# Kernel optimization log

Measured on AMD Instinct MI355X. Metric: run time of the kernel, lower is better.

Reference implementation:

```python
import jax, jax.numpy as jnp
import numpy as np
from jax import lax

POINTS = 512  # number of FPS-sampled centroids
KNN = 16      # neighbors per centroid


def setup_inputs() -> dict:
    key = jax.random.key(0)
    # [B, N, 3+C]: first 3 channels are xyz coordinates, rest are features
    x = jax.random.normal(key, (8, 16384, 16), dtype=jnp.float32)
    return {"x": x}


def _furthest_point_sample(xyz, npoint):
    """Standard FPS (seeded at index 0, as in the pointnet2 CUDA op).
    xyz: [B, N, 3] -> idx: [B, npoint] int32."""
    B, N, _ = xyz.shape

    def step(carry, _):
        min_d, last = carry
        last_pt = jnp.take_along_axis(xyz, last[:, None, None], axis=1)  # [B,1,3]
        d = jnp.sum((xyz - last_pt) ** 2, axis=-1)                        # [B,N]
        min_d = jnp.minimum(min_d, d)
        nxt = jnp.argmax(min_d, axis=-1).astype(jnp.int32)
        return (min_d, nxt), nxt

    first = jnp.zeros((B,), dtype=jnp.int32)
    init = (jnp.full((B, N), 1e10, dtype=xyz.dtype), first)
    _, rest = lax.scan(step, init, None, length=npoint - 1)  # [npoint-1, B]
    return jnp.concatenate([first[:, None], rest.T], axis=1)  # [B, npoint]


def _index_points(points, idx):
    """points: [B,N,C], idx: [B,S] or [B,S,K] -> gathered [*idx.shape, C]."""
    B = points.shape[0]
    flat = idx.reshape(B, -1)                                  # [B, S*K]
    out = jnp.take_along_axis(points, flat[:, :, None], axis=1)
    return out.reshape(*idx.shape, points.shape[-1])


def reference(x):
    # FPS over coordinates only
    idx = _furthest_point_sample(x[:, :, :3], POINTS)          # [B, P]
    sampled = _index_points(x, idx)                             # [B, P, 3+C]
    s = sampled[:, :, :3]
    p = x[:, :, :3]
    # squared euclidean distance: ||s||^2 + ||p||^2 - 2 s.p  -> [B, P, N]
    dist = (jnp.sum(s * s, axis=-1)[:, :, None]
            + jnp.sum(p * p, axis=-1)[:, None, :]
            - 2.0 * jnp.einsum('bpc,bnc->bpn', s, p))
    # full argsort then slice, matching distances.argsort()[:, :, :knn]
    knn_idx = jnp.argsort(dist, axis=-1)[:, :, :KNN]            # [B, P, K]
    return _index_points(x, knn_idx)                            # [B, P, K, 3+C]
```

## Files before the change

kernel.cpp:

```cpp
#include <hip/hip_runtime.h>
#include <hip/hip_bf16.h>
#include <stdint.h>

#define B_      8
#define N_      16384
#define NPOINT  512
#define KNN_    16
#define C_      16

__device__ __forceinline__ float fmulrn(float a, float b){ return __fmul_rn(a,b); }
__device__ __forceinline__ float faddrn(float a, float b){ return __fadd_rn(a,b); }
__device__ __forceinline__ float fsubrn(float a, float b){ return __fsub_rn(a,b); }

__device__ __forceinline__ uint32_t umax_(uint32_t a, uint32_t b){ return a > b ? a : b; }

__device__ __forceinline__ uint32_t row16_max(uint32_t x){
    uint32_t t;
    t = (uint32_t)__builtin_amdgcn_update_dpp((int)x, (int)x, 0x111, 0xf, 0xf, false); x = umax_(x, t);
    t = (uint32_t)__builtin_amdgcn_update_dpp((int)x, (int)x, 0x112, 0xf, 0xf, false); x = umax_(x, t);
    t = (uint32_t)__builtin_amdgcn_update_dpp((int)x, (int)x, 0x114, 0xf, 0xf, false); x = umax_(x, t);
    t = (uint32_t)__builtin_amdgcn_update_dpp((int)x, (int)x, 0x118, 0xf, 0xf, false); x = umax_(x, t);
    return x;
}

__device__ __forceinline__ uint32_t wave_max_uniform(uint32_t x){
    x = row16_max(x);
    uint32_t a = (uint32_t)__builtin_amdgcn_readlane((int)x, 15);
    uint32_t b = (uint32_t)__builtin_amdgcn_readlane((int)x, 31);
    uint32_t c = (uint32_t)__builtin_amdgcn_readlane((int)x, 47);
    uint32_t d = (uint32_t)__builtin_amdgcn_readlane((int)x, 63);
    return umax_(umax_(a, b), umax_(c, d));
}

__device__ __forceinline__ unsigned long long quad_max_u64(unsigned long long k){
    uint32_t lo = (uint32_t)k, hi = (uint32_t)(k >> 32);
    {
        uint32_t olo = (uint32_t)__builtin_amdgcn_update_dpp((int)lo, (int)lo, 0xB1, 0xf, 0xf, false);
        uint32_t ohi = (uint32_t)__builtin_amdgcn_update_dpp((int)hi, (int)hi, 0xB1, 0xf, 0xf, false);
        bool take = (ohi > hi) || (ohi == hi && olo > lo);
        hi = take ? ohi : hi; lo = take ? olo : lo;
    }
    {
        uint32_t olo = (uint32_t)__builtin_amdgcn_update_dpp((int)lo, (int)lo, 0x4E, 0xf, 0xf, false);
        uint32_t ohi = (uint32_t)__builtin_amdgcn_update_dpp((int)hi, (int)hi, 0x4E, 0xf, 0xf, false);
        bool take = (ohi > hi) || (ohi == hi && olo > lo);
        hi = take ? ohi : hi; lo = take ? olo : lo;
    }
    return ((unsigned long long)hi << 32) | lo;
}

__global__ void prep_kernel(const float* __restrict__ x, float4* __restrict__ pts){
    int i = blockIdx.x * blockDim.x + threadIdx.x;
    if (i >= B_ * N_) return;
    const float4* x4 = (const float4*)x;
    float4 q = x4[(size_t)i * 4];
    float p2 = faddrn(faddrn(fmulrn(q.x,q.x), fmulrn(q.y,q.y)), fmulrn(q.z,q.z));
    pts[i] = make_float4(q.x, q.y, q.z, p2);
}

#define FPS_NB   4
#define MBOX_N   (B_ * NPOINT * FPS_NB)
__global__ void zero_part_kernel(unsigned long long* __restrict__ part){
    int i = blockIdx.x * blockDim.x + threadIdx.x;
    if (i < MBOX_N) part[i] = 0ULL;
}

#define FPS_T    1024
#define FPS_NW   (FPS_T/64)
#define SLICE    (N_ / FPS_NB)
#define FOR_S4(F) F(0) F(1) F(2) F(3)

__global__ void __launch_bounds__(FPS_T)
fps_kernel_mb(const float4* __restrict__ pts, float4* __restrict__ s_out,
              unsigned long long* __restrict__ part){
    __shared__ float2   xy[SLICE];
    __shared__ uint32_t red_v[2][FPS_NW];
    __shared__ uint32_t red_i[2][FPS_NW];

    const int b    = blockIdx.x & 7;
    const int blk  = blockIdx.x >> 3;
    const int tid  = threadIdx.x;
    const int lane = tid & 63;
    const int wv   = tid >> 6;
    const int base = blk * SLICE;
    const float4* P = pts + (size_t)b * N_;
    unsigned long long* mbox = part + ((size_t)b * NPOINT) * FPS_NB;

#define DECL_S(s) float z##s, md##s;
    FOR_S4(DECL_S)
#undef DECL_S

#define INIT_S(s) { float4 q = P[base + (s) * FPS_T + tid]; \
        xy[(s) * FPS_T + tid] = make_float2(q.x, q.y); \
        z##s = q.z; md##s = 1e10f; }
    FOR_S4(INIT_S)
#undef INIT_S

    float lx, ly, lz;
    {
        float4 q0 = P[0];
        lx = q0.x; ly = q0.y; lz = q0.z;
        if (blk == 0 && tid == 0) s_out[(size_t)b * NPOINT + 0] = q0;
    }
    __syncthreads();

    for (int it = 1; it < NPOINT; ++it){
        float    bv = -1.0f;
        uint32_t bi = 0;
#define DO_S(s) { \
        float2 c = xy[(s) * FPS_T + tid]; \
        float dx = fsubrn(c.x, lx); \
        float dy = fsubrn(c.y, ly); \
        float dz = fsubrn(z##s, lz); \
        float d  = faddrn(faddrn(fmulrn(dx,dx), fmulrn(dy,dy)), fmulrn(dz,dz)); \
        md##s = fminf(md##s, d); \
        if (md##s > bv){ bv = md##s; bi = (uint32_t)(base + (s) * FPS_T + tid); } }
        FOR_S4(DO_S)
#undef DO_S

        uint32_t vb    = __float_as_uint(bv);
        uint32_t gmaxw = wave_max_uniform(vb);
        uint32_t gidxw = wave_max_uniform((vb == gmaxw) ? ~bi : 0u);
        const int par = it & 1;
        if (lane == 0){ red_v[par][wv] = gmaxw; red_i[par][wv] = gidxw; }
        __syncthreads();
        uint32_t rv = red_v[par][lane & 15];
        uint32_t ri = red_i[par][lane & 15];
        uint32_t gv = (uint32_t)__builtin_amdgcn_readlane((int)row16_max(rv), 15);
        uint32_t gn = (uint32_t)__builtin_amdgcn_readlane(
                          (int)row16_max((rv == gv) ? ri : 0u), 15);
        unsigned long long kblk = ((unsigned long long)gv << 32) | gn;

        unsigned long long* slotp = mbox + (size_t)it * FPS_NB;
        if (tid == 0)
            __hip_atomic_store(&slotp[blk], kblk, __ATOMIC_RELAXED,
                               __HIP_MEMORY_SCOPE_AGENT);
        unsigned long long v = 0;
        int guard = 0;
        for (;;){
            if (v == 0)
                v = __hip_atomic_load(&slotp[lane & 3], __ATOMIC_RELAXED,
                                      __HIP_MEMORY_SCOPE_AGENT);
            if (__all(v != 0ULL)) break;
            if (++guard > (1 << 20)) return;
        }
        unsigned long long kmax = quad_max_u64(v);
        uint32_t gi  = ~((uint32_t)kmax);
        uint32_t giu = (uint32_t)__builtin_amdgcn_readfirstlane((int)gi);
        giu &= (uint32_t)(N_ - 1);
        float4 q = P[giu];
        lx = q.x; ly = q.y; lz = q.z;
        if (blk == 0 && tid == 0) s_out[(size_t)b * NPOINT + it] = q;
    }
}

#define KT       1024
#define KNN_T    512

__global__ void __launch_bounds__(KNN_T)
__attribute__((amdgpu_waves_per_eu(4, 4)))
knn_kernel(const float* __restrict__ x,
           const float4* __restrict__ pts,
           const float4* __restrict__ s_arr,
           float* __restrict__ out){
    __shared__ float4 tile[KT];

    const int wv   = threadIdx.x >> 6;
    const int lane = threadIdx.x & 63;
    const int blk  = blockIdx.x;
    const int b    = blk >> 6;
    const int p    = ((blk & 63) << 3) | wv;

    const float4 s = s_arr[(size_t)b * NPOINT + p];
    const float sx = s.x, sy = s.y, sz = s.z, s2 = s.w;
    const float4* P = pts + (size_t)b * N_;

#define FOR_V(F) F(0) F(1) F(2) F(3) F(4) F(5) F(6) F(7) \
                 F(8) F(9) F(10) F(11) F(12) F(13) F(14) F(15)
#define DECLV(t) unsigned long long v##t = ~0ULL;
    FOR_V(DECLV)
#undef DECLV

#define PROC(q, n) { \
        float dot = faddrn(faddrn(fmulrn(sz, (q).z), fmulrn(sy, (q).y)), fmulrn(sx, (q).x)); \
        float d = fsubrn(faddrn(s2, (q).w), fmulrn(2.0f, dot)); \
        uint32_t bits = __float_as_uint(d); \
        uint32_t key  = bits ^ (((uint32_t)((int32_t)bits >> 31)) | 0x80000000u); \
        unsigned long long c = ((unsigned long long)key << 32) | (uint32_t)(n); \
        if (c < v15){ \
            bool lt0=c<v0,  lt1=c<v1,  lt2=c<v2,  lt3=c<v3; \
            bool lt4=c<v4,  lt5=c<v5,  lt6=c<v6,  lt7=c<v7; \
            bool lt8=c<v8,  lt9=c<v9,  lt10=c<v10, lt11=c<v11; \
            bool lt12=c<v12, lt13=c<v13, lt14=c<v14; \
            v15 = lt14 ? v14 : c; \
            v14 = lt14 ? (lt13 ? v13 : c) : v14; \
            v13 = lt13 ? (lt12 ? v12 : c) : v13; \
            v12 = lt12 ? (lt11 ? v11 : c) : v12; \
            v11 = lt11 ? (lt10 ? v10 : c) : v11; \
            v10 = lt10 ? (lt9  ? v9  : c) : v10; \
            v9  = lt9  ? (lt8  ? v8  : c) : v9;  \
            v8  = lt8  ? (lt7  ? v7  : c) : v8;  \
            v7  = lt7  ? (lt6  ? v6  : c) : v7;  \
            v6  = lt6  ? (lt5  ? v5  : c) : v6;  \
            v5  = lt5  ? (lt4  ? v4  : c) : v5;  \
            v4  = lt4  ? (lt3  ? v3  : c) : v4;  \
            v3  = lt3  ? (lt2  ? v2  : c) : v3;  \
            v2  = lt2  ? (lt1  ? v1  : c) : v2;  \
            v1  = lt1  ? (lt0  ? v0  : c) : v1;  \
            v0  = lt0  ? c : v0; \
        } }

    for (int t = 0; t < N_/KT; ++t){
        float4 a0 = P[t*KT + threadIdx.x];
        float4 a1 = P[t*KT + threadIdx.x + KNN_T];
        __syncthreads();
        tile[threadIdx.x]          = a0;
        tile[threadIdx.x + KNN_T]  = a1;
        __syncthreads();
        #pragma unroll 4
        for (int g = 0; g < KT/64; ++g){
            const int n = t*KT + (g << 6) + lane;
            float4 q = tile[(g << 6) + lane];
            PROC(q, n)
        }
    }
#undef PROC

    uint32_t myidx = 0;
    const int myr = lane >> 2;
    #pragma unroll 1
    for (int r = 0; r < KNN_; ++r){
        unsigned long long h = v0;
        unsigned long long g = h;
        #pragma unroll
        for (int off = 1; off < 64; off <<= 1){
            unsigned long long o = __shfl_xor(g, off, 64);
            if (o < g) g = o;
        }
        if (h == g){
            v0=v1; v1=v2; v2=v3; v3=v4; v4=v5; v5=v6; v6=v7; v7=v8;
            v8=v9; v9=v10; v10=v11; v11=v12; v12=v13; v13=v14; v14=v15;
            v15=~0ULL;
        }
        if (myr == r) myidx = (uint32_t)g;
    }
    myidx &= (uint32_t)(N_ - 1);

    const int c4 = lane & 3;
    const float4* X4 = (const float4*)x;
    float4 valq = X4[((size_t)b * N_ + myidx) * 4 + c4];
    float4* O4 = (float4*)out;
    O4[(((size_t)b * NPOINT + p) * KNN_ + myr) * 4 + c4] = valq;
}

extern "C" void kernel_launch(void* const* d_in, const int* in_sizes, int n_in,
                              void* d_out, int out_size, void* d_ws, size_t ws_size,
                              hipStream_t stream) {
    const float* x = (const float*)d_in[0];
    float* out = (float*)d_out;

    const size_t pts_bytes  = (size_t)B_ * N_ * sizeof(float4);
    const size_t s_bytes    = (size_t)B_ * NPOINT * sizeof(float4);
    const size_t part_bytes = (size_t)MBOX_N * sizeof(unsigned long long);
    if (ws_size < pts_bytes + s_bytes + part_bytes) return;
    float4* pts   = (float4*)d_ws;
    float4* s_arr = (float4*)((char*)d_ws + pts_bytes);
    unsigned long long* part =
        (unsigned long long*)((char*)d_ws + pts_bytes + s_bytes);

    prep_kernel<<<(B_*N_ + 255)/256, 256, 0, stream>>>(x, pts);
    zero_part_kernel<<<(MBOX_N + 255)/256, 256, 0, stream>>>(part);
    fps_kernel_mb<<<B_*FPS_NB, FPS_T, 0, stream>>>(pts, s_arr, part);
    knn_kernel<<<(B_*NPOINT)/8, KNN_T, 0, stream>>>(x, pts, s_arr, out);
}
```

Baseline: 1.018 ms.

## Fuse FPS and KNN into one kernel with progress-flag streaming

Merges the FPS and KNN kernels into a single launch. The first 32 blocks run FPS and publish each sampled centroid plus a per-batch progress counter with release atomics. The remaining blocks wait on that counter until their 16 centroids exist, then run the KNN top-16 scan, so KNN work overlaps the long serial FPS loop. KNN blocks grow to 1024 threads (16 centroids each), and the shared tile load is cut to one float4 per thread. Correctness depends on all FPS blocks being resident before spinning KNN blocks fill the GPU, and the larger fused block may raise register pressure for the KNN path.

Result: slower. 2.141 ms (+110.3%).

```diff
diff --git a/kernel.cpp b/kernel.cpp
--- a/kernel.cpp
+++ b/kernel.cpp
@@ -60,9 +60,10 @@
 
 #define FPS_NB   4
 #define MBOX_N   (B_ * NPOINT * FPS_NB)
+#define ZERO_N   (MBOX_N + 8)
 __global__ void zero_part_kernel(unsigned long long* __restrict__ part){
     int i = blockIdx.x * blockDim.x + threadIdx.x;
-    if (i < MBOX_N) part[i] = 0ULL;
+    if (i < ZERO_N) part[i] = 0ULL;
 }
 
 #define FPS_T    1024
@@ -70,109 +71,138 @@
 #define SLICE    (N_ / FPS_NB)
 #define FOR_S4(F) F(0) F(1) F(2) F(3)
 
-__global__ void __launch_bounds__(FPS_T)
-fps_kernel_mb(const float4* __restrict__ pts, float4* __restrict__ s_out,
-              unsigned long long* __restrict__ part){
+#define FUSE_FPS_BLOCKS (B_ * FPS_NB)
+#define KNN_RPB  16
+#define FUSE_KNN_BLOCKS (B_ * NPOINT / KNN_RPB)
+#define KT       1024
+
+__global__ void __launch_bounds__(1024, 8)
+fused_kernel(const float4* __restrict__ pts,
+             unsigned long long* __restrict__ sarr,
+             unsigned long long* __restrict__ part,
+             unsigned int* __restrict__ prog,
+             const float* __restrict__ x,
+             float* __restrict__ out){
     __shared__ float2   xy[SLICE];
     __shared__ uint32_t red_v[2][FPS_NW];
     __shared__ uint32_t red_i[2][FPS_NW];
-
-    const int b    = blockIdx.x & 7;
-    const int blk  = blockIdx.x >> 3;
+    __shared__ float4   tile[KT];
+
     const int tid  = threadIdx.x;
     const int lane = tid & 63;
     const int wv   = tid >> 6;
-    const int base = blk * SLICE;
-    const float4* P = pts + (size_t)b * N_;
-    unsigned long long* mbox = part + ((size_t)b * NPOINT) * FPS_NB;
+
+    if (blockIdx.x < FUSE_FPS_BLOCKS){
+        const int b    = blockIdx.x & 7;
+        const int blk  = blockIdx.x >> 3;
+        const int base = blk * SLICE;
+        const float4* P = pts + (size_t)b * N_;
+        unsigned long long* mbox = part + ((size_t)b * NPOINT) * FPS_NB;
 
 #define DECL_S(s) float z##s, md##s;
-    FOR_S4(DECL_S)
+        FOR_S4(DECL_S)
 #undef DECL_S
 
 #define INIT_S(s) { float4 q = P[base + (s) * FPS_T + tid]; \
         xy[(s) * FPS_T + tid] = make_float2(q.x, q.y); \
         z##s = q.z; md##s = 1e10f; }
-    FOR_S4(INIT_S)
+        FOR_S4(INIT_S)
 #undef INIT_S
 
-    float lx, ly, lz;
-    {
-        float4 q0 = P[0];
-        lx = q0.x; ly = q0.y; lz = q0.z;
-        if (blk == 0 && tid == 0) s_out[(size_t)b * NPOINT + 0] = q0;
+        float lx, ly, lz;
+        {
+            float4 q0 = P[0];
+            lx = q0.x; ly = q0.y; lz = q0.z;
+            if (blk == 0 && tid == 0){
+                unsigned long long w0 = ((unsigned long long)__float_as_uint(q0.y) << 32) | __float_as_uint(q0.x);
+                unsigned long long w1 = ((unsigned long long)__float_as_uint(q0.w) << 32) | __float_as_uint(q0.z);
+                __hip_atomic_store(&sarr[0 + ((size_t)b * NPOINT) * 2], w0, __ATOMIC_RELAXED, __HIP_MEMORY_SCOPE_AGENT);
+                __hip_atomic_store(&sarr[1 + ((size_t)b * NPOINT) * 2], w1, __ATOMIC_RELAXED, __HIP_MEMORY_SCOPE_AGENT);
+                __hip_atomic_store(&prog[b], 1u, __ATOMIC_RELEASE, __HIP_MEMORY_SCOPE_AGENT);
+            }
+        }
+        __syncthreads();
+
+        for (int it = 1; it < NPOINT; ++it){
+            float    bv = -1.0f;
+            uint32_t bi = 0;
+#define DO_S(s) { \
+            float2 c = xy[(s) * FPS_T + tid]; \
+            float dx = fsubrn(c.x, lx); \
+            float dy = fsubrn(c.y, ly); \
+            float dz = fsubrn(z##s, lz); \
+            float d  = faddrn(faddrn(fmulrn(dx,dx), fmulrn(dy,dy)), fmulrn(dz,dz)); \
+            md##s = fminf(md##s, d); \
+            if (md##s > bv){ bv = md##s; bi = (uint32_t)(base + (s) * FPS_T + tid); } }
+            FOR_S4(DO_S)
+#undef DO_S
+
+            uint32_t vb    = __float_as_uint(bv);
+            uint32_t gmaxw = wave_max_uniform(vb);
+            uint32_t gidxw = wave_max_uniform((vb == gmaxw) ? ~bi : 0u);
+            const int par = it & 1;
+            if (lane == 0){ red_v[par][wv] = gmaxw; red_i[par][wv] = gidxw; }
+            __syncthreads();
+            uint32_t rv = red_v[par][lane & 15];
+            uint32_t ri = red_i[par][lane & 15];
+            uint32_t gv = (uint32_t)__builtin_amdgcn_readlane((int)row16_max(rv), 15);
+            uint32_t gn = (uint32_t)__builtin_amdgcn_readlane(
+                              (int)row16_max((rv == gv) ? ri : 0u), 15);
+            unsigned long long kblk = ((unsigned long long)gv << 32) | gn;
+
+            unsigned long long* slotp = mbox + (size_t)it * FPS_NB;
+            if (tid == 0)
+                __hip_atomic_store(&slotp[blk], kblk, __ATOMIC_RELAXED,
+                                   __HIP_MEMORY_SCOPE_AGENT);
+            unsigned long long v = 0;
+            int guard = 0;
+            for (;;){
+                if (v == 0)
+                    v = __hip_atomic_load(&slotp[lane & 3], __ATOMIC_RELAXED,
+                                          __HIP_MEMORY_SCOPE_AGENT);
+                if (__all(v != 0ULL)) break;
+                if (++guard > (1 << 20)) return;
+            }
+            unsigned long long kmax = quad_max_u64(v);
+            uint32_t gi  = ~((uint32_t)kmax);
+            uint32_t giu = (uint32_t)__builtin_amdgcn_readfirstlane((int)gi);
+            giu &= (uint32_t)(N_ - 1);
+            float4 q = P[giu];
+            lx = q.x; ly = q.y; lz = q.z;
+            if (blk == 0 && tid == 0){
+                unsigned long long w0 = ((unsigned long long)__float_as_uint(q.y) << 32) | __float_as_uint(q.x);
+                unsigned long long w1 = ((unsigned long long)__float_as_uint(q.w) << 32) | __float_as_uint(q.z);
+                size_t sb = ((size_t)b * NPOINT + it) * 2;
+                __hip_atomic_store(&sarr[sb + 0], w0, __ATOMIC_RELAXED, __HIP_MEMORY_SCOPE_AGENT);
+                __hip_atomic_store(&sarr[sb + 1], w1, __ATOMIC_RELAXED, __HIP_MEMORY_SCOPE_AGENT);
+                __hip_atomic_store(&prog[b], (unsigned int)(it + 1), __ATOMIC_RELEASE, __HIP_MEMORY_SCOPE_AGENT);
+            }
+        }
+        return;
+    }
+
+    const int kb   = blockIdx.x - FUSE_FPS_BLOCKS;
+    const int b    = kb >> 5;
+    const int rowb = (kb & 31) << 4;
+    const int p    = rowb + wv;
+
+    if (tid == 0){
+        int guard = 0;
+        while (__hip_atomic_load(&prog[b], __ATOMIC_ACQUIRE,
+                                 __HIP_MEMORY_SCOPE_AGENT) < (unsigned int)(rowb + KNN_RPB)){
+            __builtin_amdgcn_s_sleep(8);
+            if (++guard > (1 << 20)) break;
+        }
     }
     __syncthreads();
 
-    for (int it = 1; it < NPOINT; ++it){
-        float    bv = -1.0f;
-        uint32_t bi = 0;
-#define DO_S(s) { \
-        float2 c = xy[(s) * FPS_T + tid]; \
-        float dx = fsubrn(c.x, lx); \
-        float dy = fsubrn(c.y, ly); \
-        float dz = fsubrn(z##s, lz); \
-        float d  = faddrn(faddrn(fmulrn(dx,dx), fmulrn(dy,dy)), fmulrn(dz,dz)); \
-        md##s = fminf(md##s, d); \
-        if (md##s > bv){ bv = md##s; bi = (uint32_t)(base + (s) * FPS_T + tid); } }
-        FOR_S4(DO_S)
-#undef DO_S
-
-        uint32_t vb    = __float_as_uint(bv);
-        uint32_t gmaxw = wave_max_uniform(vb);
-        uint32_t gidxw = wave_max_uniform((vb == gmaxw) ? ~bi : 0u);
-        const int par = it & 1;
-        if (lane == 0){ red_v[par][wv] = gmaxw; red_i[par][wv] = gidxw; }
-        __syncthreads();
-        uint32_t rv = red_v[par][lane & 15];
-        uint32_t ri = red_i[par][lane & 15];
-        uint32_t gv = (uint32_t)__builtin_amdgcn_readlane((int)row16_max(rv), 15);
-        uint32_t gn = (uint32_t)__builtin_amdgcn_readlane(
-                          (int)row16_max((rv == gv) ? ri : 0u), 15);
-        unsigned long long kblk = ((unsigned long long)gv << 32) | gn;
-
-        unsigned long long* slotp = mbox + (size_t)it * FPS_NB;
-        if (tid == 0)
-            __hip_atomic_store(&slotp[blk], kblk, __ATOMIC_RELAXED,
-                               __HIP_MEMORY_SCOPE_AGENT);
-        unsigned long long v = 0;
-        int guard = 0;
-        for (;;){
-            if (v == 0)
-                v = __hip_atomic_load(&slotp[lane & 3], __ATOMIC_RELAXED,
-                                      __HIP_MEMORY_SCOPE_AGENT);
-            if (__all(v != 0ULL)) break;
-            if (++guard > (1 << 20)) return;
-        }
-        unsigned long long kmax = quad_max_u64(v);
-        uint32_t gi  = ~((uint32_t)kmax);
-        uint32_t giu = (uint32_t)__builtin_amdgcn_readfirstlane((int)gi);
-        giu &= (uint32_t)(N_ - 1);
-        float4 q = P[giu];
-        lx = q.x; ly = q.y; lz = q.z;
-        if (blk == 0 && tid == 0) s_out[(size_t)b * NPOINT + it] = q;
-    }
-}
-
-#define KT       1024
-#define KNN_T    512
-
-__global__ void __launch_bounds__(KNN_T)
-__attribute__((amdgpu_waves_per_eu(4, 4)))
-knn_kernel(const float* __restrict__ x,
-           const float4* __restrict__ pts,
-           const float4* __restrict__ s_arr,
-           float* __restrict__ out){
-    __shared__ float4 tile[KT];
-
-    const int wv   = threadIdx.x >> 6;
-    const int lane = threadIdx.x & 63;
-    const int blk  = blockIdx.x;
-    const int b    = blk >> 6;
-    const int p    = ((blk & 63) << 3) | wv;
-
-    const float4 s = s_arr[(size_t)b * NPOINT + p];
-    const float sx = s.x, sy = s.y, sz = s.z, s2 = s.w;
+    size_t sb = ((size_t)b * NPOINT + p) * 2;
+    unsigned long long w0 = __hip_atomic_load(&sarr[sb + 0], __ATOMIC_RELAXED, __HIP_MEMORY_SCOPE_AGENT);
+    unsigned long long w1 = __hip_atomic_load(&sarr[sb + 1], __ATOMIC_RELAXED, __HIP_MEMORY_SCOPE_AGENT);
+    const float sx = __uint_as_float((uint32_t)w0);
+    const float sy = __uint_as_float((uint32_t)(w0 >> 32));
+    const float sz = __uint_as_float((uint32_t)w1);
+    const float s2 = __uint_as_float((uint32_t)(w1 >> 32));
     const float4* P = pts + (size_t)b * N_;
 
 #define FOR_V(F) F(0) F(1) F(2) F(3) F(4) F(5) F(6) F(7) \
@@ -211,11 +241,9 @@
         } }
 
     for (int t = 0; t < N_/KT; ++t){
-        float4 a0 = P[t*KT + threadIdx.x];
-        float4 a1 = P[t*KT + threadIdx.x + KNN_T];
+        float4 a0 = P[t*KT + tid];
         __syncthreads();
-        tile[threadIdx.x]          = a0;
-        tile[threadIdx.x + KNN_T]  = a1;
+        tile[tid] = a0;
         __syncthreads();
         #pragma unroll 4
         for (int g = 0; g < KT/64; ++g){
@@ -260,16 +288,17 @@
     float* out = (float*)d_out;
 
     const size_t pts_bytes  = (size_t)B_ * N_ * sizeof(float4);
-    const size_t s_bytes    = (size_t)B_ * NPOINT * sizeof(float4);
-    const size_t part_bytes = (size_t)MBOX_N * sizeof(unsigned long long);
+    const size_t s_bytes    = (size_t)B_ * NPOINT * 2 * sizeof(unsigned long long);
+    const size_t part_bytes = (size_t)ZERO_N * sizeof(unsigned long long);
     if (ws_size < pts_bytes + s_bytes + part_bytes) return;
-    float4* pts   = (float4*)d_ws;
-    float4* s_arr = (float4*)((char*)d_ws + pts_bytes);
+    float4* pts = (float4*)d_ws;
+    unsigned long long* sarr = (unsigned long long*)((char*)d_ws + pts_bytes);
     unsigned long long* part =
         (unsigned long long*)((char*)d_ws + pts_bytes + s_bytes);
+    unsigned int* prog = (unsigned int*)(part + MBOX_N);
 
     prep_kernel<<<(B_*N_ + 255)/256, 256, 0, stream>>>(x, pts);
-    zero_part_kernel<<<(MBOX_N + 255)/256, 256, 0, stream>>>(part);
-    fps_kernel_mb<<<B_*FPS_NB, FPS_T, 0, stream>>>(pts, s_arr, part);
-    knn_kernel<<<(B_*NPOINT)/8, KNN_T, 0, stream>>>(x, pts, s_arr, out);
-}
+    zero_part_kernel<<<(ZERO_N + 255)/256, 256, 0, stream>>>(part);
+    fused_kernel<<<FUSE_FPS_BLOCKS + FUSE_KNN_BLOCKS, 1024, 0, stream>>>(
+        pts, sarr, part, prog, x, out);
+}
```
